# Kernel optimization log

Measured on AMD Instinct MI355X. Metric: run time of the kernel, lower is better.

Reference implementation:

```python
import jax, jax.numpy as jnp
import numpy as np

B, T, D = 64, 512, 768
H = D // 2      # per-direction LSTM hidden
L = 33          # num_labels


def setup_inputs() -> dict:
    key = jax.random.key(0)
    ks = jax.random.split(key, 14)
    input_embed = jax.random.normal(ks[0], (B, T, D), dtype=jnp.float32)
    # pack_padded_sequence requires lengths sorted in decreasing order
    lengths = jnp.sort(jax.random.randint(ks[1], (B,), T // 2, T + 1))[::-1]
    lengths = lengths.at[0].set(T)
    mask = jnp.arange(T)[None, :] < lengths[:, None]          # [B,T] bool
    labels = jax.random.randint(ks[2], (B, T), 0, L, dtype=jnp.int32)
    index = jax.random.randint(ks[3], (B, 2), 0, T)
    s = 0.1
    w_ih_f = jax.random.normal(ks[4], (4 * H, D), jnp.float32) * s
    w_hh_f = jax.random.normal(ks[5], (4 * H, H), jnp.float32) * s
    b_f = jax.random.normal(ks[6], (4 * H,), jnp.float32) * s
    w_ih_b = jax.random.normal(ks[7], (4 * H, D), jnp.float32) * s
    w_hh_b = jax.random.normal(ks[8], (4 * H, H), jnp.float32) * s
    b_b = jax.random.normal(ks[9], (4 * H,), jnp.float32) * s
    lin_w = jax.random.normal(ks[10], (L, 2 * H), jnp.float32) * s
    lin_b = jnp.zeros((L,), jnp.float32)
    trans = jax.random.normal(ks[11], (L, L), jnp.float32) * s
    start_trans = jax.random.normal(ks[12], (L,), jnp.float32) * s
    end_trans = jax.random.normal(ks[13], (L,), jnp.float32) * s
    return dict(input_embed=input_embed, mask=mask, labels=labels, index=index,
                w_ih_f=w_ih_f, w_hh_f=w_hh_f, b_f=b_f,
                w_ih_b=w_ih_b, w_hh_b=w_hh_b, b_b=b_b,
                lin_w=lin_w, lin_b=lin_b,
                trans=trans, start_trans=start_trans, end_trans=end_trans)


def _run_lstm(x, mask_f, w_ih, w_hh, b):
    """Unidirectional LSTM over packed (length-masked) sequences.
    Output is zero at padded steps; state is frozen past each sequence length.
    x: [B,T,D] -> [B,T,H]. Torch gate order: i, f, g, o.
    """
    xp = jnp.einsum('btd,gd->btg', x, w_ih) + b          # [B,T,4H] precomputed
    xp_t = xp.transpose(1, 0, 2)                         # [T,B,4H]
    m_t = mask_f.T[:, :, None]                           # [T,B,1]
    nH = w_hh.shape[1]
    init = (jnp.zeros((x.shape[0], nH), x.dtype), jnp.zeros((x.shape[0], nH), x.dtype))

    def step(carry, inp):
        h, c = carry
        xg, m = inp
        g = xg + h @ w_hh.T
        i, f, gc, o = jnp.split(g, 4, axis=-1)
        c_new = jax.nn.sigmoid(f) * c + jax.nn.sigmoid(i) * jnp.tanh(gc)
        h_new = jax.nn.sigmoid(o) * jnp.tanh(c_new)
        carry = (jnp.where(m > 0, h_new, h), jnp.where(m > 0, c_new, c))
        return carry, h_new * m

    _, ys = jax.lax.scan(step, init, (xp_t, m_t))
    return ys.transpose(1, 0, 2)


def reference(input_embed, mask, labels, index,
              w_ih_f, w_hh_f, b_f, w_ih_b, w_hh_b, b_b,
              lin_w, lin_b, trans, start_trans, end_trans):
    mask_f = mask.astype(input_embed.dtype)              # [B,T]
    lengths = mask.sum(1).astype(jnp.int32)              # [B]

    # BiLSTM with pack_padded semantics (dropout in eval mode = identity)
    h_fwd = _run_lstm(input_embed, mask_f, w_ih_f, w_hh_f, b_f)
    # reverse within each sequence's valid region (involution on valid steps)
    rev_idx = jnp.clip(lengths[:, None] - 1 - jnp.arange(T)[None, :], 0, T - 1)
    x_rev = jnp.take_along_axis(input_embed, rev_idx[..., None], axis=1)
    h_b_rev = _run_lstm(x_rev, mask_f, w_ih_b, w_hh_b, b_b)
    h_bwd = jnp.take_along_axis(h_b_rev, rev_idx[..., None], axis=1) * mask_f[..., None]
    h = jnp.concatenate([h_fwd, h_bwd], axis=-1)         # [B,T,2H]

    # emissions, masked as in the original (out *= mask.unsqueeze(-1))
    em = (jnp.einsum('bth,lh->btl', h, lin_w) + lin_b) * mask_f[..., None]

    # ---- CRF log-likelihood: numerator (gold path score) ----
    em_y = jnp.take_along_axis(em, labels[..., None], axis=2)[..., 0]   # [B,T]
    tr = trans[labels[:, :-1], labels[:, 1:]]                            # [B,T-1]
    num = start_trans[labels[:, 0]] + em_y[:, 0] \
        + jnp.sum((tr + em_y[:, 1:]) * mask_f[:, 1:], axis=1)
    last_y = jnp.take_along_axis(labels, (lengths - 1)[:, None], axis=1)[:, 0]
    num = num + end_trans[last_y]

    # ---- CRF log-partition: forward algorithm scan ----
    alpha0 = start_trans[None, :] + em[:, 0]             # [B,L]

    def step(alpha, inp):
        e_t, m_t = inp                                   # [B,L], [B]
        new = jax.nn.logsumexp(alpha[:, :, None] + trans[None, :, :] + e_t[:, None, :], axis=1)
        return jnp.where(m_t[:, None] > 0, new, alpha), None

    alpha, _ = jax.lax.scan(step, alpha0,
                            (em[:, 1:].transpose(1, 0, 2), mask_f[:, 1:].T))
    logZ = jax.nn.logsumexp(alpha + end_trans[None, :], axis=1)

    score = num - logZ                                   # per-sample log-likelihood
    return -jnp.mean(score)
```

## Files before the change

### kernel.cpp

```cpp
#include <hip/hip_runtime.h>

typedef unsigned short U16;
typedef unsigned int   U32;
typedef unsigned long long U64;
typedef __attribute__((ext_vector_type(8))) short S8;
typedef __attribute__((ext_vector_type(4))) float F4;

#define B_  64
#define T_  512
#define DD  768
#define HH  384
#define G4  1536
#define NL  33

__device__ __forceinline__ U16 f2bf(float f){
  U32 u = __float_as_uint(f);
  u += 0x7fffu + ((u >> 16) & 1u);
  return (U16)(u >> 16);
}
__device__ __forceinline__ float bf2f(U16 h){ return __uint_as_float(((U32)h) << 16); }
__device__ __forceinline__ float frcp(float x){
  float r;
  asm("v_rcp_f32 %0, %1" : "=v"(r) : "v"(x));
  return r;
}
__device__ __forceinline__ float sigm(float x){
  return frcp(1.f + __expf(-x));
}
__device__ __forceinline__ float tanh_(float x){
  float e = __expf(2.f * x);
  return 1.f - 2.f * frcp(e + 1.f);
}

__global__ void k_pre(const U32* mask, int* lens,
                      const float* wf_, const float* wb_, const float* lw_,
                      const float* bfv, const float* bbv,
                      U16* wcat, U16* lwb, float* bcat){
  int blk = blockIdx.x;
  int tid = threadIdx.x;
  if (blk < 64){
    if (tid < 64){
      int b = blk, l = tid;
      bool b32 = (mask[0] == 1u);
      int cnt = 0;
      for (int t = l; t < T_; t += 64){
        int v = b32 ? ((const int*)mask)[b * T_ + t]
                    : (int)((const unsigned char*)mask)[b * T_ + t];
        cnt += (v != 0);
      }
      #pragma unroll
      for (int o = 32; o >= 1; o >>= 1) cnt += __shfl_xor(cnt, o);
      if (l == 0) lens[b] = cnt;
    }
    return;
  }
  const int WE = G4 * DD;
  const int LWE = NL * DD;
  int total = 2 * WE + LWE + 2 * G4;
  for (int i = (blk - 64) * 256 + tid; i < total; i += 512 * 256){
    if (i < WE) wcat[i] = f2bf(wf_[i]);
    else if (i < 2 * WE) wcat[i] = f2bf(wb_[i - WE]);
    else if (i < 2 * WE + LWE) lwb[i - 2 * WE] = f2bf(lw_[i - 2 * WE]);
    else { int j = i - 2 * WE - LWE; bcat[j] = (j < G4) ? bfv[j] : bbv[j - G4]; }
  }
}

__global__ __launch_bounds__(256) void k_gemm(const float* __restrict__ x,
                                              const U16* __restrict__ Bw,
                                              const float* __restrict__ bias, U16* C){
  __shared__ __align__(16) U16 As[128 * 64];
  __shared__ __align__(16) U16 Bs[128 * 64];
  int swz = (blockIdx.x & 7) * 768 + (blockIdx.x >> 3);
  int mb = swz & 255, nb = swz >> 8;
  int m0 = mb * 128, n0 = nb * 128;
  int tid = threadIdx.x;
  int w = tid >> 6, l = tid & 63;
  int lr = l & 15, lk = (l >> 4) * 8;
  int wm = (w >> 1) * 64, wn = (w & 1) * 64;
  int srow = tid >> 3;
  int scol = (tid & 7) * 8;
  F4 acc[4][4];
  #pragma unroll
  for (int i = 0; i < 4; i++)
    #pragma unroll
    for (int j = 0; j < 4; j++) acc[i][j] = (F4){0.f, 0.f, 0.f, 0.f};

  for (int kt = 0; kt < DD; kt += 64){
    __syncthreads();
    #pragma unroll
    for (int r = 0; r < 4; r++){
      int row = r * 32 + srow;
      int sw = scol ^ ((row & 7) * 8);
      const float* ap = x + (size_t)(m0 + row) * DD + kt + sw;
      float4 v0 = *(const float4*)ap;
      float4 v1 = *(const float4*)(ap + 4);
      S8 t;
      t[0] = (short)f2bf(v0.x); t[1] = (short)f2bf(v0.y);
      t[2] = (short)f2bf(v0.z); t[3] = (short)f2bf(v0.w);
      t[4] = (short)f2bf(v1.x); t[5] = (short)f2bf(v1.y);
      t[6] = (short)f2bf(v1.z); t[7] = (short)f2bf(v1.w);
      *(S8*)&As[row * 64 + sw] = t;
      __builtin_amdgcn_global_load_lds((const U32*)(Bw + (size_t)(n0 + row) * DD + kt + sw),
                                       (U32*)(Bs + row * 64 + scol), 16, 0, 0);
    }
    __syncthreads();
    #pragma unroll
    for (int kk = 0; kk < 64; kk += 32){
      S8 af[4], bf[4];
      int cs = (kk + lk) ^ ((lr & 7) * 8);
      #pragma unroll
      for (int i = 0; i < 4; i++) af[i] = *(const S8*)(As + (wm + i * 16 + lr) * 64 + cs);
      #pragma unroll
      for (int i = 0; i < 4; i++) bf[i] = *(const S8*)(Bs + (wn + i * 16 + lr) * 64 + cs);
      #pragma unroll
      for (int i = 0; i < 4; i++)
        #pragma unroll
        for (int j = 0; j < 4; j++)
          acc[i][j] = __builtin_amdgcn_mfma_f32_16x16x32_bf16(af[i], bf[j], acc[i][j], 0, 0, 0);
    }
  }
  #pragma unroll
  for (int j = 0; j < 4; j++){
    int col = n0 + wn + j * 16 + lr;
    float bv = bias[col];
    #pragma unroll
    for (int i = 0; i < 4; i++){
      #pragma unroll
      for (int rg = 0; rg < 4; rg++){
        int row = m0 + wm + i * 16 + (l >> 4) * 4 + rg;
        C[(size_t)row * 3072 + col] = f2bf(acc[i][j][rg] + bv);
      }
    }
  }
}

__global__ __launch_bounds__(256, 1) void k_rec(const U16* __restrict__ xp,
                                                const float* __restrict__ whf,
                                                const float* __restrict__ whb,
                                                const int* __restrict__ len_,
                                                U16* __restrict__ hcat, U64* hx){
  int blk = blockIdx.x;
  int g = blk & 7, m = blk >> 3;
  int dir = g >> 2, chunk = g & 3, sb = chunk * 16;
  const float* wh = dir ? whb : whf;
  int tid = threadIdx.x;
  int w = tid >> 6, l = tid & 63;
  int lr = l & 15, lq = l >> 4;
  int jloc = m * 64 + w * 16 + lr;

  S8 wf[4][12];
  #pragma unroll
  for (int q = 0; q < 4; q++){
    #pragma unroll
    for (int kc = 0; kc < 12; kc++){
      const float* p = wh + (size_t)(q * HH + jloc) * HH + kc * 32 + lq * 8;
      float4 v0 = *(const float4*)p;
      float4 v1 = *(const float4*)(p + 4);
      S8 t;
      t[0] = (short)f2bf(v0.x); t[1] = (short)f2bf(v0.y); t[2] = (short)f2bf(v0.z); t[3] = (short)f2bf(v0.w);
      t[4] = (short)f2bf(v1.x); t[5] = (short)f2bf(v1.y); t[6] = (short)f2bf(v1.z); t[7] = (short)f2bf(v1.w);
      wf[q][kc] = t;
    }
  }

  __shared__ __align__(16) U16 hl[16][408];
  for (int i = tid; i < 16 * 408; i += 256) ((U16*)hl)[i] = 0;
  int lens[4];
  #pragma unroll
  for (int r = 0; r < 4; r++) lens[r] = len_[sb + lq * 4 + r];
  int steps = len_[sb];
  float cst[4] = {0.f, 0.f, 0.f, 0.f}, hst[4] = {0.f, 0.f, 0.f, 0.f};
  __syncthreads();

  for (int step = 0; step < steps; ++step){
    float xv[4][4];
    #pragma unroll
    for (int r = 0; r < 4; r++){
      int L = lens[r];
      int t = dir ? (L - 1 - step) : step;
      if (t < 0) t = 0;
      size_t basei = ((size_t)(sb + lq * 4 + r) * T_ + t) * 3072 + dir * G4;
      #pragma unroll
      for (int q = 0; q < 4; q++) xv[q][r] = bf2f(xp[basei + q * HH + jloc]);
    }
    if (step){
      const U64* src = hx + (size_t)((step & 1) * 8 + g) * 3072;
      U64 v[12];
      #pragma unroll
      for (int k = 0; k < 12; k++)
        v[k] = __hip_atomic_load(src + tid + k * 256, __ATOMIC_RELAXED, __HIP_MEMORY_SCOPE_AGENT);
      U32 expct = (U32)step;
      while (true){
        U32 bad = 0;
        #pragma unroll
        for (int k = 0; k < 12; k++) bad |= (((U32)(v[k] >> 32)) != expct) ? (1u << k) : 0u;
        if (!bad) break;
        #pragma unroll
        for (int k = 0; k < 12; k++)
          if (bad & (1u << k))
            v[k] = __hip_atomic_load(src + tid + k * 256, __ATOMIC_RELAXED, __HIP_MEMORY_SCOPE_AGENT);
      }
      #pragma unroll
      for (int k = 0; k < 12; k++){
        int wi = tid + k * 256;
        int col = wi >> 3, p = wi & 7;
        U32 lo = (U32)v[k];
        hl[2 * p + 0][col] = (U16)lo;
        hl[2 * p + 1][col] = (U16)(lo >> 16);
      }
      __syncthreads();
    }
    F4 acc[4];
    #pragma unroll
    for (int q = 0; q < 4; q++) acc[q] = (F4){0.f, 0.f, 0.f, 0.f};
    #pragma unroll
    for (int kc = 0; kc < 12; kc++){
      S8 a = *(const S8*)&hl[lr][kc * 32 + lq * 8];
      #pragma unroll
      for (int q = 0; q < 4; q++)
        acc[q] = __builtin_amdgcn_mfma_f32_16x16x32_bf16(a, wf[q][kc], acc[q], 0, 0, 0);
    }
    #pragma unroll
    for (int r = 0; r < 4; r++){
      float ip = acc[0][r] + xv[0][r];
      float fp = acc[1][r] + xv[1][r];
      float gp = acc[2][r] + xv[2][r];
      float op = acc[3][r] + xv[3][r];
      float cn = sigm(fp) * cst[r] + sigm(ip) * tanh_(gp);
      float hn = sigm(op) * tanh_(cn);
      if (step < lens[r]){ cst[r] = cn; hst[r] = hn; }
    }
    {
      U64 tag = ((U64)(U32)(step + 1)) << 32;
      U64 w0 = (U64)((U32)f2bf(hst[0]) | ((U32)f2bf(hst[1]) << 16)) | tag;
      U64 w1 = (U64)((U32)f2bf(hst[2]) | ((U32)f2bf(hst[3]) << 16)) | tag;
      U64* dst = hx + (size_t)(((step + 1) & 1) * 8 + g) * 3072 + jloc * 8 + lq * 2;
      __hip_atomic_store(dst + 0, w0, __ATOMIC_RELAXED, __HIP_MEMORY_SCOPE_AGENT);
      __hip_atomic_store(dst + 1, w1, __ATOMIC_RELAXED, __HIP_MEMORY_SCOPE_AGENT);
    }
    #pragma unroll
    for (int r = 0; r < 4; r++){
      if (step < lens[r]){
        int t = dir ? (lens[r] - 1 - step) : step;
        hcat[((size_t)(sb + lq * 4 + r) * T_ + t) * (2 * HH) + dir * HH + jloc] = f2bf(hst[r]);
      }
    }
  }
}

__global__ __launch_bounds__(256) void k_em(const U16* hcat, const U16* lwb, const float* lin_b, float* em){
  __shared__ __align__(16) U16 lw[NL * DD];
  __shared__ __align__(16) U16 hs[32 * DD];
  int tid = threadIdx.x;
  for (int i = tid; i < NL * DD / 4; i += 256) ((U64*)lw)[i] = ((const U64*)lwb)[i];
  size_t r0 = (size_t)blockIdx.x * 32;
  const U64* hsrc = (const U64*)(hcat + r0 * DD);
  for (int i = tid; i < 32 * DD / 4; i += 256) ((U64*)hs)[i] = hsrc[i];
  __syncthreads();
  for (int e = tid; e < 32 * NL; e += 256){
    int rr = e / NL, ll = e % NL;
    const U16* hp = &hs[rr * DD];
    const U16* wp = &lw[ll * DD];
    float s = 0.f;
    #pragma unroll 8
    for (int k = 0; k < DD; k += 2){
      U32 hv = *(const U32*)&hp[k];
      U32 wv = *(const U32*)&wp[k];
      s = fmaf(__uint_as_float(hv << 16), __uint_as_float(wv << 16), s);
      s = fmaf(__uint_as_float(hv & 0xffff0000u), __uint_as_float(wv & 0xffff0000u), s);
    }
    em[(r0 + rr) * NL + ll] = s + lin_b[ll];
  }
}

__global__ void k_crf(const float* em, const int* labels, const int* len_, const float* trans,
                      const float* startt, const float* endt, float* score){
  int b = blockIdx.x, l = threadIdx.x;
  int L = len_[b];
  const int* lab = labels + b * T_;
  const float* emb = em + (size_t)b * T_ * NL;
  float part = 0.f;
  for (int t = 1 + l; t < L; t += 64){
    int lp = lab[t - 1], lc = lab[t];
    part += trans[lp * NL + lc] + emb[(size_t)t * NL + lc];
  }
  #pragma unroll
  for (int o = 32; o >= 1; o >>= 1) part += __shfl_xor(part, o);
  float num = part + startt[lab[0]] + emb[lab[0]] + endt[lab[L - 1]];
  bool act = l < NL;
  int jj = act ? l : (NL - 1);
  float tc[NL];
  #pragma unroll
  for (int i = 0; i < NL; i++) tc[i] = trans[i * NL + jj];
  float a = startt[jj] + emb[jj];
  for (int t = 1; t < L; ++t){
    float vv[NL];
    float mx = -3.0e38f;
    #pragma unroll
    for (int i = 0; i < NL; i++){ vv[i] = __shfl(a, i) + tc[i]; mx = fmaxf(mx, vv[i]); }
    float s = 0.f;
    #pragma unroll
    for (int i = 0; i < NL; i++) s += __expf(vv[i] - mx);
    a = mx + __logf(s) + emb[(size_t)t * NL + jj];
  }
  float val = act ? (a + endt[jj]) : -3.0e38f;
  float mx = val;
  #pragma unroll
  for (int o = 32; o >= 1; o >>= 1) mx = fmaxf(mx, __shfl_xor(mx, o));
  float se = __expf(val - mx);
  #pragma unroll
  for (int o = 32; o >= 1; o >>= 1) se += __shfl_xor(se, o);
  float logZ = mx + __logf(se);
  if (l == 0) score[b] = num - logZ;
}

__global__ void k_final(const float* score, float* out){
  int l = threadIdx.x;
  float v = score[l];
  #pragma unroll
  for (int o = 32; o >= 1; o >>= 1) v += __shfl_xor(v, o);
  if (l == 0) out[0] = -v / 64.f;
}

__global__ void k_sentinel(float* out){ out[0] = -12345.f; }

extern "C" void kernel_launch(void* const* d_in, const int* in_sizes, int n_in,
                              void* d_out, int out_size, void* d_ws, size_t ws_size,
                              hipStream_t stream){
  const float* x      = (const float*)d_in[0];
  const void*  mask   = d_in[1];
  const int*   labels = (const int*)d_in[2];
  const float* w_ih_f = (const float*)d_in[4];
  const float* w_hh_f = (const float*)d_in[5];
  const float* b_f    = (const float*)d_in[6];
  const float* w_ih_b = (const float*)d_in[7];
  const float* w_hh_b = (const float*)d_in[8];
  const float* b_b    = (const float*)d_in[9];
  const float* lin_w  = (const float*)d_in[10];
  const float* lin_b  = (const float*)d_in[11];
  const float* trans  = (const float*)d_in[12];
  const float* startt = (const float*)d_in[13];
  const float* endt   = (const float*)d_in[14];
  float* out = (float*)d_out;

  const size_t WS_NEEDED = 261158912;
  if (ws_size < WS_NEEDED){
    k_sentinel<<<1, 1, 0, stream>>>(out);
    return;
  }

  char* ws = (char*)d_ws;
  size_t off = 0;
  auto take = [&](size_t bytes) -> char* {
    char* p = ws + off;
    off += (bytes + 255) & ~(size_t)255;
    return p;
  };
  U16*  xp    = (U16*)take((size_t)32768 * 3072 * 2);
  U16*  hcat  = (U16*)take((size_t)32768 * 768 * 2);
  U16*  wcat  = (U16*)take((size_t)3072 * 768 * 2);
  U16*  lwb   = (U16*)take((size_t)NL * 768 * 2);
  float* bcat = (float*)take(3072 * 4);
  int*  lens  = (int*)take(256);
  U64*  hx    = (U64*)take((size_t)2 * 8 * 3072 * 8);
  float* em   = (float*)take((size_t)32768 * NL * 4);
  float* score= (float*)take(256);

  (void)hipMemsetAsync(hx, 0, (size_t)2 * 8 * 3072 * 8, stream);
  k_pre<<<576, 256, 0, stream>>>((const U32*)mask, lens,
                                 w_ih_f, w_ih_b, lin_w, b_f, b_b, wcat, lwb, bcat);
  k_gemm<<<6144, 256, 0, stream>>>(x, wcat, bcat, xp);
  k_rec<<<48, 256, 0, stream>>>(xp, w_hh_f, w_hh_b, lens, hcat, hx);
  k_em<<<1024, 256, 0, stream>>>(hcat, lwb, lin_b, em);
  k_crf<<<64, 64, 0, stream>>>(em, labels, lens, trans, startt, endt, score);
  k_final<<<1, 64, 0, stream>>>(score, out);
}
```

Baseline: 2.368 ms.

## Pre-convert input to bf16 once and tune recurrence spin-wait barrier

```diff
diff --git a/kernel.cpp b/kernel.cpp
--- a/kernel.cpp
+++ b/kernel.cpp
@@ -32,7 +32,7 @@
   return 1.f - 2.f * frcp(e + 1.f);
 }
 
-__global__ void k_pre(const U32* mask, int* lens,
+__global__ void k_pre(const float* x, U64* xb, const U32* mask, int* lens,
                       const float* wf_, const float* wb_, const float* lw_,
                       const float* bfv, const float* bbv,
                       U16* wcat, U16* lwb, float* bcat){
@@ -54,18 +54,27 @@
     }
     return;
   }
-  const int WE = G4 * DD;
-  const int LWE = NL * DD;
-  int total = 2 * WE + LWE + 2 * G4;
-  for (int i = (blk - 64) * 256 + tid; i < total; i += 512 * 256){
-    if (i < WE) wcat[i] = f2bf(wf_[i]);
-    else if (i < 2 * WE) wcat[i] = f2bf(wb_[i - WE]);
-    else if (i < 2 * WE + LWE) lwb[i - 2 * WE] = f2bf(lw_[i - 2 * WE]);
-    else { int j = i - 2 * WE - LWE; bcat[j] = (j < G4) ? bfv[j] : bbv[j - G4]; }
-  }
-}
-
-__global__ __launch_bounds__(256) void k_gemm(const float* __restrict__ x,
+  if (blk < 1088){
+    const int WE = G4 * DD;
+    const int LWE = NL * DD;
+    int total = 2 * WE + LWE + 2 * G4;
+    for (int i = (blk - 64) * 256 + tid; i < total; i += 1024 * 256){
+      if (i < WE) wcat[i] = f2bf(wf_[i]);
+      else if (i < 2 * WE) wcat[i] = f2bf(wb_[i - WE]);
+      else if (i < 2 * WE + LWE) lwb[i - 2 * WE] = f2bf(lw_[i - 2 * WE]);
+      else { int j = i - 2 * WE - LWE; bcat[j] = (j < G4) ? bfv[j] : bbv[j - G4]; }
+    }
+    return;
+  }
+  size_t n4 = (size_t)B_ * T_ * DD / 4;
+  for (size_t i = (size_t)(blk - 1088) * 256 + tid; i < n4; i += (size_t)2048 * 256){
+    float4 v = ((const float4*)x)[i];
+    U64 o = (U64)f2bf(v.x) | ((U64)f2bf(v.y) << 16) | ((U64)f2bf(v.z) << 32) | ((U64)f2bf(v.w) << 48);
+    xb[i] = o;
+  }
+}
+
+__global__ __launch_bounds__(256) void k_gemm(const U16* __restrict__ A,
                                               const U16* __restrict__ Bw,
                                               const float* __restrict__ bias, U16* C){
   __shared__ __align__(16) U16 As[128 * 64];
@@ -91,15 +100,8 @@
     for (int r = 0; r < 4; r++){
       int row = r * 32 + srow;
       int sw = scol ^ ((row & 7) * 8);
-      const float* ap = x + (size_t)(m0 + row) * DD + kt + sw;
-      float4 v0 = *(const float4*)ap;
-      float4 v1 = *(const float4*)(ap + 4);
-      S8 t;
-      t[0] = (short)f2bf(v0.x); t[1] = (short)f2bf(v0.y);
-      t[2] = (short)f2bf(v0.z); t[3] = (short)f2bf(v0.w);
-      t[4] = (short)f2bf(v1.x); t[5] = (short)f2bf(v1.y);
-      t[6] = (short)f2bf(v1.z); t[7] = (short)f2bf(v1.w);
-      *(S8*)&As[row * 64 + sw] = t;
+      __builtin_amdgcn_global_load_lds((const U32*)(A + (size_t)(m0 + row) * DD + kt + sw),
+                                       (U32*)(As + row * 64 + scol), 16, 0, 0);
       __builtin_amdgcn_global_load_lds((const U32*)(Bw + (size_t)(n0 + row) * DD + kt + sw),
                                        (U32*)(Bs + row * 64 + scol), 16, 0, 0);
     }
@@ -184,6 +186,7 @@
       for (int q = 0; q < 4; q++) xv[q][r] = bf2f(xp[basei + q * HH + jloc]);
     }
     if (step){
+      __builtin_amdgcn_s_sleep(10);
       const U64* src = hx + (size_t)((step & 1) * 8 + g) * 3072;
       U64 v[12];
       #pragma unroll
@@ -208,7 +211,10 @@
         hl[2 * p + 0][col] = (U16)lo;
         hl[2 * p + 1][col] = (U16)(lo >> 16);
       }
-      __syncthreads();
+      asm volatile("s_waitcnt lgkmcnt(0)" ::: "memory");
+      __builtin_amdgcn_s_barrier();
+      asm volatile("" ::: "memory");
+      __builtin_amdgcn_sched_barrier(0);
     }
     F4 acc[4];
     #pragma unroll
@@ -365,11 +371,12 @@
   U64*  hx    = (U64*)take((size_t)2 * 8 * 3072 * 8);
   float* em   = (float*)take((size_t)32768 * NL * 4);
   float* score= (float*)take(256);
+  U16*  xbf   = hcat;
 
   (void)hipMemsetAsync(hx, 0, (size_t)2 * 8 * 3072 * 8, stream);
-  k_pre<<<576, 256, 0, stream>>>((const U32*)mask, lens,
-                                 w_ih_f, w_ih_b, lin_w, b_f, b_b, wcat, lwb, bcat);
-  k_gemm<<<6144, 256, 0, stream>>>(x, wcat, bcat, xp);
+  k_pre<<<3136, 256, 0, stream>>>(x, (U64*)xbf, (const U32*)mask, lens,
+                                  w_ih_f, w_ih_b, lin_w, b_f, b_b, wcat, lwb, bcat);
+  k_gemm<<<6144, 256, 0, stream>>>(xbf, wcat, bcat, xp);
   k_rec<<<48, 256, 0, stream>>>(xp, w_hh_f, w_hh_b, lens, hcat, hx);
   k_em<<<1024, 256, 0, stream>>>(hcat, lwb, lin_b, em);
   k_crf<<<64, 64, 0, stream>>>(em, labels, lens, trans, startt, endt, score);
```

Result: faster. 2.152 ms (-9.1%).
